# Optimization experiments

Hardware: AMD Instinct MI355X
Metric: run time of the kernel (lower is better)

The kernel has to match this reference:

```python
import jax, jax.numpy as jnp
import numpy as np

ALPHA = 0.1
EPS = 1e-8


def setup_inputs() -> dict:
    key = jax.random.key(0)
    k1, k2, k3 = jax.random.split(key, 3)
    B, C, F = 2048, 256, 256
    feat = jax.random.normal(k1, (B, F), dtype=jnp.float32)
    labels = jax.random.randint(k2, (B,), 0, C, dtype=jnp.int64)
    means = jax.random.normal(k3, (C, F), dtype=jnp.float32)
    vars_ = jnp.ones((C, F), dtype=jnp.float32)
    return {"feat": feat, "labels": labels, "means": means, "vars_": vars_}


def reference(feat, labels, means, vars_):
    C = means.shape[0]
    inv_v = 1.0 / (vars_ + EPS)                      # [C,F]
    # Mahalanobis distance via GEMM decomposition instead of [B,C,F] tensor:
    m_distance = 0.5 * (
        jnp.einsum('bf,cf->bc', feat * feat, inv_v)
        - 2.0 * jnp.einsum('bf,cf->bc', feat, means * inv_v)
        + jnp.sum(means * means * inv_v, axis=1)      # [C]
    )                                                 # [B,C]
    onehot = jax.nn.one_hot(labels, C, dtype=m_distance.dtype)  # [B,C]
    adjust_m_distance = m_distance + onehot * ALPHA * m_distance
    det = jnp.prod(vars_, axis=1)                     # [C] det of diagonal cov
    probability = jnp.exp(-adjust_m_distance) / (det * det + EPS)  # [B,C]
    class_probability = jnp.sum(onehot * probability, axis=1)       # [B]
    classification_loss = -jnp.log(
        class_probability / (jnp.sum(probability, axis=1) + EPS) + EPS
    )                                                 # [B]
    return (classification_loss, means, vars_)
```

## Files before the change

### kernel.cpp

```cpp
#include <hip/hip_runtime.h>
#include <math.h>

#define ALPHA 0.1f
#define EPS 1e-8f

constexpr int B = 2048;
constexpr int C = 256;
constexpr int F = 256;
constexpr int TB = 8;

__global__ __launch_bounds__(256) void prep_kernel(
    const float* __restrict__ means, const float* __restrict__ vars_,
    float* __restrict__ ivq, float* __restrict__ mvq,
    float* __restrict__ msq, float* __restrict__ invden,
    float* __restrict__ out_means, float* __restrict__ out_vars)
{
    const int c = blockIdx.x;
    const int f = threadIdx.x;
    const float v = vars_[c * F + f];
    const float m = means[c * F + f];
    const float iv = 1.0f / (v + EPS);

    const int idx = (f >> 2) * (C * 4) + c * 4 + (f & 3);
    ivq[idx] = iv;
    mvq[idx] = m * iv;

    out_means[c * F + f] = m;
    out_vars[c * F + f]  = v;

    float s = m * m * iv;
    float p = v;
    #pragma unroll
    for (int off = 32; off > 0; off >>= 1) {
        s += __shfl_down(s, off);
        p *= __shfl_down(p, off);
    }
    __shared__ float ss[4], pp[4];
    const int wave = f >> 6, lane = f & 63;
    if (lane == 0) { ss[wave] = s; pp[wave] = p; }
    __syncthreads();
    if (f == 0) {
        const float st = ss[0] + ss[1] + ss[2] + ss[3];
        const float pt = pp[0] * pp[1] * pp[2] * pp[3];
        msq[c]    = st;
        invden[c] = 1.0f / (pt * pt + EPS);
    }
}

__global__ __launch_bounds__(256) void lgm_main(
    const float* __restrict__ feat, const int* __restrict__ labels,
    const float* __restrict__ ivq, const float* __restrict__ mvq,
    const float* __restrict__ msq, const float* __restrict__ invden,
    float* __restrict__ loss)
{
    __shared__ float sfeat[TB][F];
    __shared__ int   slab[TB];
    __shared__ float wsum[TB][4];
    __shared__ float cls[TB];

    const int tid = threadIdx.x;
    const int b0  = blockIdx.x * TB;

    #pragma unroll
    for (int i = 0; i < TB; ++i)
        sfeat[i][tid] = feat[(b0 + i) * F + tid];
    if (tid < TB) { slab[tid] = labels[b0 + tid]; cls[tid] = 0.0f; }
    __syncthreads();

    float acc[TB];
    #pragma unroll
    for (int i = 0; i < TB; ++i) acc[i] = 0.0f;

    const float4* __restrict__ iv4p = (const float4*)ivq;
    const float4* __restrict__ mv4p = (const float4*)mvq;

    for (int f4 = 0; f4 < F / 4; ++f4) {
        const float4 iv = iv4p[f4 * C + tid];
        const float4 mv = mv4p[f4 * C + tid];
        #pragma unroll
        for (int j = 0; j < 4; ++j) {
            const float ivj = (&iv.x)[j];
            const float mv2 = -2.0f * (&mv.x)[j];
            #pragma unroll
            for (int i = 0; i < TB; ++i) {
                const float x = sfeat[i][f4 * 4 + j];
                acc[i] = fmaf(x, fmaf(ivj, x, mv2), acc[i]);
            }
        }
    }

    const float mq  = msq[tid];
    const float idn = invden[tid];
    float pv[TB];
    #pragma unroll
    for (int i = 0; i < TB; ++i) {
        const float dist = 0.5f * (acc[i] + mq);
        const float adj  = (slab[i] == tid) ? dist * (1.0f + ALPHA) : dist;
        pv[i] = expf(-adj) * idn;
    }

    const int lane = tid & 63, wave = tid >> 6;
    #pragma unroll
    for (int i = 0; i < TB; ++i) {
        float s = pv[i];
        #pragma unroll
        for (int off = 32; off > 0; off >>= 1) s += __shfl_down(s, off);
        if (lane == 0) wsum[i][wave] = s;
        if (slab[i] == tid) cls[i] = pv[i];
    }
    __syncthreads();

    if (tid < TB) {
        const float s = wsum[tid][0] + wsum[tid][1] + wsum[tid][2] + wsum[tid][3];
        loss[b0 + tid] = -logf(cls[tid] / (s + EPS) + EPS);
    }
}

extern "C" void kernel_launch(void* const* d_in, const int* in_sizes, int n_in,
                              void* d_out, int out_size, void* d_ws, size_t ws_size,
                              hipStream_t stream) {
    const float* feat   = (const float*)d_in[0];
    const int*   labels = (const int*)  d_in[1];
    const float* means  = (const float*)d_in[2];
    const float* vars_  = (const float*)d_in[3];

    float* out       = (float*)d_out;
    float* loss      = out;
    float* out_means = out + B;
    float* out_vars  = out + B + C * F;

    float* ws     = (float*)d_ws;
    float* ivq    = ws;
    float* mvq    = ivq + C * F;
    float* msq    = mvq + C * F;
    float* invden = msq + C;

    prep_kernel<<<C, 256, 0, stream>>>(means, vars_, ivq, mvq, msq, invden,
                                       out_means, out_vars);
    lgm_main<<<B / TB, 256, 0, stream>>>(feat, labels, ivq, mvq, msq, invden, loss);
}
```

Measured before the change: 80.46 us.

## Split feature reduction across two thread halves with 512-thread blocks

The main kernel now launches 512 threads per block, and each half handles half of the feature dimension for the same 256 classes. Partial sums are combined through shared memory before the exp/normalization step. The -2 scale is folded into the precomputed mean/var table, and feature rows are read as float4 from shared memory. This is meant to raise parallelism and cut the serial loop length per thread. In exchange it adds two block barriers and leaves half of the threads idle during the epilogue.

```diff
diff --git a/kernel.cpp b/kernel.cpp
--- a/kernel.cpp
+++ b/kernel.cpp
@@ -8,6 +8,8 @@
 constexpr int C = 256;
 constexpr int F = 256;
 constexpr int TB = 8;
+constexpr int NF4 = F / 4;
+constexpr int HALF_F4 = NF4 / 2;
 
 __global__ __launch_bounds__(256) void prep_kernel(
     const float* __restrict__ means, const float* __restrict__ vars_,
@@ -23,7 +25,7 @@
 
     const int idx = (f >> 2) * (C * 4) + c * 4 + (f & 3);
     ivq[idx] = iv;
-    mvq[idx] = m * iv;
+    mvq[idx] = -2.0f * m * iv;
 
     out_means[c * F + f] = m;
     out_vars[c * F + f]  = v;
@@ -47,7 +49,7 @@
     }
 }
 
-__global__ __launch_bounds__(256) void lgm_main(
+__global__ __launch_bounds__(512) void lgm_main(
     const float* __restrict__ feat, const int* __restrict__ labels,
     const float* __restrict__ ivq, const float* __restrict__ mvq,
     const float* __restrict__ msq, const float* __restrict__ invden,
@@ -56,15 +58,15 @@
     __shared__ float sfeat[TB][F];
     __shared__ int   slab[TB];
     __shared__ float wsum[TB][4];
-    __shared__ float cls[TB];
+    __shared__ float clsp[TB];
 
-    const int tid = threadIdx.x;
-    const int b0  = blockIdx.x * TB;
+    const int tid  = threadIdx.x;
+    const int cls  = tid & (C - 1);
+    const int half = tid >> 8;
+    const int b0   = blockIdx.x * TB;
 
-    #pragma unroll
-    for (int i = 0; i < TB; ++i)
-        sfeat[i][tid] = feat[(b0 + i) * F + tid];
-    if (tid < TB) { slab[tid] = labels[b0 + tid]; cls[tid] = 0.0f; }
+    ((float4*)sfeat)[tid] = ((const float4*)(feat + b0 * F))[tid];
+    if (tid < TB) { slab[tid] = labels[b0 + tid]; clsp[tid] = 0.0f; }
     __syncthreads();
 
     float acc[TB];
@@ -74,45 +76,59 @@
     const float4* __restrict__ iv4p = (const float4*)ivq;
     const float4* __restrict__ mv4p = (const float4*)mvq;
 
-    for (int f4 = 0; f4 < F / 4; ++f4) {
-        const float4 iv = iv4p[f4 * C + tid];
-        const float4 mv = mv4p[f4 * C + tid];
+    #pragma unroll 4
+    for (int k = 0; k < HALF_F4; ++k) {
+        const int f4 = half * HALF_F4 + k;
+        const float4 iv = iv4p[f4 * C + cls];
+        const float4 mv = mv4p[f4 * C + cls];
         #pragma unroll
-        for (int j = 0; j < 4; ++j) {
-            const float ivj = (&iv.x)[j];
-            const float mv2 = -2.0f * (&mv.x)[j];
-            #pragma unroll
-            for (int i = 0; i < TB; ++i) {
-                const float x = sfeat[i][f4 * 4 + j];
-                acc[i] = fmaf(x, fmaf(ivj, x, mv2), acc[i]);
-            }
+        for (int i = 0; i < TB; ++i) {
+            const float4 x = *(const float4*)&sfeat[i][f4 * 4];
+            float a = acc[i];
+            a = fmaf(x.x, fmaf(iv.x, x.x, mv.x), a);
+            a = fmaf(x.y, fmaf(iv.y, x.y, mv.y), a);
+            a = fmaf(x.z, fmaf(iv.z, x.z, mv.z), a);
+            a = fmaf(x.w, fmaf(iv.w, x.w, mv.w), a);
+            acc[i] = a;
         }
     }
 
-    const float mq  = msq[tid];
-    const float idn = invden[tid];
+    __syncthreads();
+    if (half == 1) {
+        #pragma unroll
+        for (int i = 0; i < TB; ++i) sfeat[i][cls] = acc[i];
+    }
+    __syncthreads();
+
     float pv[TB];
-    #pragma unroll
-    for (int i = 0; i < TB; ++i) {
-        const float dist = 0.5f * (acc[i] + mq);
-        const float adj  = (slab[i] == tid) ? dist * (1.0f + ALPHA) : dist;
-        pv[i] = expf(-adj) * idn;
+    const int lane = tid & 63, wave = tid >> 6;
+    if (half == 0) {
+        const float mq  = msq[cls];
+        const float idn = invden[cls];
+        #pragma unroll
+        for (int i = 0; i < TB; ++i) {
+            const float dist = 0.5f * (acc[i] + sfeat[i][cls] + mq);
+            const float adj  = (slab[i] == cls) ? dist * (1.0f + ALPHA) : dist;
+            pv[i] = expf(-adj) * idn;
+            if (slab[i] == cls) clsp[i] = pv[i];
+        }
+    } else {
+        #pragma unroll
+        for (int i = 0; i < TB; ++i) pv[i] = 0.0f;
     }
 
-    const int lane = tid & 63, wave = tid >> 6;
     #pragma unroll
     for (int i = 0; i < TB; ++i) {
         float s = pv[i];
         #pragma unroll
         for (int off = 32; off > 0; off >>= 1) s += __shfl_down(s, off);
-        if (lane == 0) wsum[i][wave] = s;
-        if (slab[i] == tid) cls[i] = pv[i];
+        if (half == 0 && lane == 0) wsum[i][wave] = s;
     }
     __syncthreads();
 
     if (tid < TB) {
         const float s = wsum[tid][0] + wsum[tid][1] + wsum[tid][2] + wsum[tid][3];
-        loss[b0 + tid] = -logf(cls[tid] / (s + EPS) + EPS);
+        loss[b0 + tid] = -logf(clsp[tid] / (s + EPS) + EPS);
     }
 }
 
@@ -137,5 +153,5 @@
 
     prep_kernel<<<C, 256, 0, stream>>>(means, vars_, ivq, mvq, msq, invden,
                                        out_means, out_vars);
-    lgm_main<<<B / TB, 256, 0, stream>>>(feat, labels, ivq, mvq, msq, invden, loss);
+    lgm_main<<<B / TB, 512, 0, stream>>>(feat, labels, ivq, mvq, msq, invden, loss);
 }
```

Measured after the change: 79.16 us (median of 2 runs). About the same (-1.6%).
